# Kernel optimization log

Measured on AMD Instinct MI355X. Metric: run time of the kernel, lower is better.

Reference implementation:

```python
import jax, jax.numpy as jnp
import numpy as np

N = 100000      # num_nodes (num_users + num_items)
E = 1600000     # directed edges after symmetrization
DIN = 256
HID = 64
DOUT = 64


def setup_inputs() -> dict:
    key = jax.random.key(0)
    k = jax.random.split(key, 4)
    x = jax.random.normal(k[0], (N, DIN), dtype=jnp.float32)
    edge_index = jax.random.randint(k[1], (2, E), 0, N)
    edge_weight = jnp.ones((E,), dtype=jnp.float32)
    W1 = jax.random.normal(k[2], (DIN, HID), dtype=jnp.float32) * (1.0 / np.sqrt(DIN))
    b1 = jnp.zeros((HID,), dtype=jnp.float32)
    W2 = jax.random.normal(k[3], (HID, DOUT), dtype=jnp.float32) * (1.0 / np.sqrt(HID))
    b2 = jnp.zeros((DOUT,), dtype=jnp.float32)
    return {"x": x, "edge_index": edge_index, "edge_weight": edge_weight,
            "W1": W1, "b1": b1, "W2": W2, "b2": b2}


def _gcn_layer(x, W, b, src, dst, ew):
    # PyG GCNConv: h = x @ W; symmetric degree normalization; scatter-add at dst; + bias
    h = x @ W                                             # [N, D_out]
    deg = jax.ops.segment_sum(ew, dst, num_segments=N)    # in-degree w.r.t. edge weights
    dinv = jnp.where(deg > 0, jax.lax.rsqrt(deg), 0.0)    # deg^{-1/2}, inf -> 0
    norm = dinv[src] * ew * dinv[dst]                     # [E_tot]
    msg = h[src] * norm[:, None]                          # gather + scale
    out = jax.ops.segment_sum(msg, dst, num_segments=N)   # scatter-add
    return out + b


def reference(x, edge_index, edge_weight, W1, b1, W2, b2):
    # add self-loops with weight 1 (GCNConv default add_self_loops=True)
    loop = jnp.arange(N, dtype=edge_index.dtype)
    src = jnp.concatenate([edge_index[0], loop])
    dst = jnp.concatenate([edge_index[1], loop])
    ew = jnp.concatenate([edge_weight, jnp.ones((N,), edge_weight.dtype)])
    h = jax.nn.relu(_gcn_layer(x, W1, b1, src, dst, ew))
    return _gcn_layer(h, W2, b2, src, dst, ew)
```

## Files before the change

### kernel.cpp

```cpp
#include <hip/hip_runtime.h>
#include <math.h>


#define GCN_DIN 256
#define GCN_HID 64
#define SCAN_B 1024

__global__ void count_kernel(const int* __restrict__ dst, int* __restrict__ counts, int E) {
    int e = blockIdx.x * blockDim.x + threadIdx.x;
    if (e < E) atomicAdd(&counts[dst[e]], 1);
}

__global__ __launch_bounds__(SCAN_B) void scan_reduce_kernel(
    const int* __restrict__ counts, int* __restrict__ blockSums, int N)
{
    __shared__ int red[SCAN_B];
    int t = threadIdx.x;
    int i = blockIdx.x * SCAN_B + t;
    red[t] = (i < N) ? counts[i] : 0;
    __syncthreads();
    #pragma unroll
    for (int off = SCAN_B / 2; off > 0; off >>= 1) {
        if (t < off) red[t] += red[t + off];
        __syncthreads();
    }
    if (t == 0) blockSums[blockIdx.x] = red[0];
}

__global__ __launch_bounds__(128) void scan_sums_kernel(
    const int* __restrict__ blockSums, int* __restrict__ blockOff,
    int* __restrict__ rowptr, int B, int N)
{
    __shared__ int s[128];
    int t = threadIdx.x;
    int v = (t < B) ? blockSums[t] : 0;
    s[t] = v;
    __syncthreads();
    #pragma unroll
    for (int off = 1; off < 128; off <<= 1) {
        int a = (t >= off) ? s[t - off] : 0;
        __syncthreads();
        s[t] += a;
        __syncthreads();
    }
    if (t < B) blockOff[t] = s[t] - v;
    if (t == B - 1) rowptr[N] = s[t];
}

__global__ __launch_bounds__(SCAN_B) void scan_final_kernel(
    const int* __restrict__ counts, const int* __restrict__ blockOff,
    int* __restrict__ rowptr, int* __restrict__ cursor, int N)
{
    __shared__ int s[SCAN_B];
    int t = threadIdx.x;
    int i = blockIdx.x * SCAN_B + t;
    int v = (i < N) ? counts[i] : 0;
    s[t] = v;
    __syncthreads();
    for (int off = 1; off < SCAN_B; off <<= 1) {
        int a = (t >= off) ? s[t - off] : 0;
        __syncthreads();
        s[t] += a;
        __syncthreads();
    }
    if (i < N) {
        int excl = blockOff[blockIdx.x] + s[t] - v;
        rowptr[i] = excl;
        cursor[i] = excl;
    }
}

__global__ void reorder_kernel(const int* __restrict__ src, const int* __restrict__ dst,
                               const float* __restrict__ ew, int* __restrict__ cursor,
                               int2* __restrict__ comb, int E) {
    int e = blockIdx.x * blockDim.x + threadIdx.x;
    if (e < E) {
        int d = dst[e];
        int pos = atomicAdd(&cursor[d], 1);
        comb[pos] = make_int2(src[e], __float_as_int(ew[e]));
    }
}

__global__ void degw_kernel(const int* __restrict__ rowptr, const int2* __restrict__ comb,
                            float* __restrict__ dinv, int N) {
    int n = blockIdx.x * blockDim.x + threadIdx.x;
    if (n >= N) return;
    float s = 1.0f;
    int je = rowptr[n + 1];
    for (int j = rowptr[n]; j < je; ++j) s += __int_as_float(comb[j].y);
    dinv[n] = (s > 0.f) ? (1.0f / sqrtf(s)) : 0.f;
}

__global__ __launch_bounds__(256) void gemm1_kernel(
    const float* __restrict__ x, const float* __restrict__ W,
    const float* __restrict__ dinv, float* __restrict__ g, int N)
{
    __shared__ float xs[32][68];
    __shared__ float ws[32][64];
    const int tid = threadIdx.x;
    const int tx = tid & 15;
    const int ty = tid >> 4;
    const int row0 = blockIdx.x * 64;

    float acc[4][4];
    #pragma unroll
    for (int i = 0; i < 4; ++i)
        #pragma unroll
        for (int j = 0; j < 4; ++j) acc[i][j] = 0.f;

    for (int k0 = 0; k0 < GCN_DIN; k0 += 32) {
        {
            int kc = tid & 7;
            int r  = tid >> 3;
            #pragma unroll
            for (int h = 0; h < 2; ++h) {
                int rr = r + 32 * h;
                int row = row0 + rr;
                float4 v = make_float4(0.f, 0.f, 0.f, 0.f);
                if (row < N) v = *(const float4*)&x[(size_t)row * GCN_DIN + k0 + kc * 4];
                xs[kc * 4 + 0][rr] = v.x;
                xs[kc * 4 + 1][rr] = v.y;
                xs[kc * 4 + 2][rr] = v.z;
                xs[kc * 4 + 3][rr] = v.w;
            }
        }
        {
            int c  = tid & 63;
            int kr = tid >> 6;
            #pragma unroll
            for (int h = 0; h < 8; ++h)
                ws[kr + 4 * h][c] = W[(size_t)(k0 + kr + 4 * h) * 64 + c];
        }
        __syncthreads();
        #pragma unroll
        for (int kk = 0; kk < 32; ++kk) {
            float4 a = *(const float4*)&xs[kk][ty * 4];
            float4 b = *(const float4*)&ws[kk][tx * 4];
            float av[4] = {a.x, a.y, a.z, a.w};
            float bv[4] = {b.x, b.y, b.z, b.w};
            #pragma unroll
            for (int i = 0; i < 4; ++i)
                #pragma unroll
                for (int j = 0; j < 4; ++j)
                    acc[i][j] = fmaf(av[i], bv[j], acc[i][j]);
        }
        __syncthreads();
    }
    #pragma unroll
    for (int i = 0; i < 4; ++i) {
        int row = row0 + ty * 4 + i;
        if (row < N) {
            float dv = dinv[row];
            float4 o = make_float4(dv * acc[i][0], dv * acc[i][1],
                                   dv * acc[i][2], dv * acc[i][3]);
            *(float4*)&g[(size_t)row * 64 + tx * 4] = o;
        }
    }
}

__global__ __launch_bounds__(256) void gemm2_kernel(
    const float* __restrict__ acc1, const float* __restrict__ W,
    const float* __restrict__ dinv, const float* __restrict__ b1,
    float* __restrict__ g, int N)
{
    __shared__ float xs[32][68];
    __shared__ float ws[32][64];
    const int tid = threadIdx.x;
    const int tx = tid & 15;
    const int ty = tid >> 4;
    const int row0 = blockIdx.x * 64;

    float acc[4][4];
    #pragma unroll
    for (int i = 0; i < 4; ++i)
        #pragma unroll
        for (int j = 0; j < 4; ++j) acc[i][j] = 0.f;

    for (int k0 = 0; k0 < GCN_HID; k0 += 32) {
        {
            int kc = tid & 7;
            int r  = tid >> 3;
            float4 bb = *(const float4*)&b1[k0 + kc * 4];
            #pragma unroll
            for (int h = 0; h < 2; ++h) {
                int rr = r + 32 * h;
                int row = row0 + rr;
                float4 v = make_float4(0.f, 0.f, 0.f, 0.f);
                if (row < N) {
                    float dv = dinv[row];
                    float4 hh = *(const float4*)&acc1[(size_t)row * 64 + k0 + kc * 4];
                    v.x = fmaxf(dv * hh.x + bb.x, 0.f);
                    v.y = fmaxf(dv * hh.y + bb.y, 0.f);
                    v.z = fmaxf(dv * hh.z + bb.z, 0.f);
                    v.w = fmaxf(dv * hh.w + bb.w, 0.f);
                }
                xs[kc * 4 + 0][rr] = v.x;
                xs[kc * 4 + 1][rr] = v.y;
                xs[kc * 4 + 2][rr] = v.z;
                xs[kc * 4 + 3][rr] = v.w;
            }
        }
        {
            int c  = tid & 63;
            int kr = tid >> 6;
            #pragma unroll
            for (int h = 0; h < 8; ++h)
                ws[kr + 4 * h][c] = W[(size_t)(k0 + kr + 4 * h) * 64 + c];
        }
        __syncthreads();
        #pragma unroll
        for (int kk = 0; kk < 32; ++kk) {
            float4 a = *(const float4*)&xs[kk][ty * 4];
            float4 b = *(const float4*)&ws[kk][tx * 4];
            float av[4] = {a.x, a.y, a.z, a.w};
            float bv[4] = {b.x, b.y, b.z, b.w};
            #pragma unroll
            for (int i = 0; i < 4; ++i)
                #pragma unroll
                for (int j = 0; j < 4; ++j)
                    acc[i][j] = fmaf(av[i], bv[j], acc[i][j]);
        }
        __syncthreads();
    }
    #pragma unroll
    for (int i = 0; i < 4; ++i) {
        int row = row0 + ty * 4 + i;
        if (row < N) {
            float dv = dinv[row];
            float4 o = make_float4(dv * acc[i][0], dv * acc[i][1],
                                   dv * acc[i][2], dv * acc[i][3]);
            *(float4*)&g[(size_t)row * 64 + tx * 4] = o;
        }
    }
}

__global__ __launch_bounds__(256) void pull_kernel(
    const int* __restrict__ rowptr, const int2* __restrict__ comb,
    const float* __restrict__ g, float* __restrict__ out, int N)
{
    int wid  = (blockIdx.x * blockDim.x + threadIdx.x) >> 6;
    int lane = threadIdx.x & 63;
    if (wid >= N) return;
    int jb = rowptr[wid], je = rowptr[wid + 1];
    float acc = g[(size_t)wid * 64 + lane];
    int j = jb;
    for (; j + 3 < je; j += 4) {
        int2 e0 = comb[j], e1 = comb[j + 1], e2 = comb[j + 2], e3 = comb[j + 3];
        float v0 = g[(size_t)e0.x * 64 + lane];
        float v1 = g[(size_t)e1.x * 64 + lane];
        float v2 = g[(size_t)e2.x * 64 + lane];
        float v3 = g[(size_t)e3.x * 64 + lane];
        acc = fmaf(__int_as_float(e0.y), v0, acc);
        acc = fmaf(__int_as_float(e1.y), v1, acc);
        acc = fmaf(__int_as_float(e2.y), v2, acc);
        acc = fmaf(__int_as_float(e3.y), v3, acc);
    }
    for (; j < je; ++j) {
        int2 e0 = comb[j];
        acc = fmaf(__int_as_float(e0.y), g[(size_t)e0.x * 64 + lane], acc);
    }
    out[(size_t)wid * 64 + lane] = acc;
}

__global__ __launch_bounds__(256) void pull_final_kernel(
    const int* __restrict__ rowptr, const int2* __restrict__ comb,
    const float* __restrict__ g, const float* __restrict__ dinv,
    const float* __restrict__ b2, float* __restrict__ out, int N)
{
    int wid  = (blockIdx.x * blockDim.x + threadIdx.x) >> 6;
    int lane = threadIdx.x & 63;
    if (wid >= N) return;
    int jb = rowptr[wid], je = rowptr[wid + 1];
    float acc = g[(size_t)wid * 64 + lane];
    int j = jb;
    for (; j + 3 < je; j += 4) {
        int2 e0 = comb[j], e1 = comb[j + 1], e2 = comb[j + 2], e3 = comb[j + 3];
        float v0 = g[(size_t)e0.x * 64 + lane];
        float v1 = g[(size_t)e1.x * 64 + lane];
        float v2 = g[(size_t)e2.x * 64 + lane];
        float v3 = g[(size_t)e3.x * 64 + lane];
        acc = fmaf(__int_as_float(e0.y), v0, acc);
        acc = fmaf(__int_as_float(e1.y), v1, acc);
        acc = fmaf(__int_as_float(e2.y), v2, acc);
        acc = fmaf(__int_as_float(e3.y), v3, acc);
    }
    for (; j < je; ++j) {
        int2 e0 = comb[j];
        acc = fmaf(__int_as_float(e0.y), g[(size_t)e0.x * 64 + lane], acc);
    }
    out[(size_t)wid * 64 + lane] = dinv[wid] * acc + b2[lane];
}

extern "C" void kernel_launch(void* const* d_in, const int* in_sizes, int n_in,
                              void* d_out, int out_size, void* d_ws, size_t ws_size,
                              hipStream_t stream) {
    const float* x  = (const float*)d_in[0];
    const int*   ei = (const int*)  d_in[1];
    const float* ew = (const float*)d_in[2];
    const float* W1 = (const float*)d_in[3];
    const float* b1 = (const float*)d_in[4];
    const float* W2 = (const float*)d_in[5];
    const float* b2 = (const float*)d_in[6];
    float* out = (float*)d_out;

    const int N = in_sizes[0] / GCN_DIN;
    const int E = in_sizes[1] / 2;
    const int* src = ei;
    const int* dst = ei + E;

    char* p = (char*)d_ws;
    int2*  comb   = (int2*)p;  p += (size_t)E * sizeof(int2);
    float* B1     = (float*)p; p += (size_t)N * 64 * sizeof(float);
    float* B2     = (float*)p; p += (size_t)N * 64 * sizeof(float);
    float* dinv   = (float*)p; p += (size_t)N * sizeof(float);
    int*   counts = (int*)p;   p += (size_t)N * sizeof(int);
    int*   cursor = (int*)p;   p += (size_t)N * sizeof(int);
    int*   rowptr = (int*)p;   p += (size_t)(N + 1) * sizeof(int);
    int*   blockSums = (int*)p; p += 128 * sizeof(int);
    int*   blockOff  = (int*)p; p += 128 * sizeof(int);

    const int eBlocks = (E + 255) / 256;
    const int gBlocks = (N + 63) / 64;
    const int wBlocks = (N + 3) / 4;
    const int sBlocks = (N + SCAN_B - 1) / SCAN_B;

    hipMemsetAsync(counts, 0, (size_t)N * sizeof(int), stream);
    count_kernel<<<eBlocks, 256, 0, stream>>>(dst, counts, E);
    scan_reduce_kernel<<<sBlocks, SCAN_B, 0, stream>>>(counts, blockSums, N);
    scan_sums_kernel<<<1, 128, 0, stream>>>(blockSums, blockOff, rowptr, sBlocks, N);
    scan_final_kernel<<<sBlocks, SCAN_B, 0, stream>>>(counts, blockOff, rowptr, cursor, N);
    reorder_kernel<<<eBlocks, 256, 0, stream>>>(src, dst, ew, cursor, comb, E);
    degw_kernel<<<(N + 255) / 256, 256, 0, stream>>>(rowptr, comb, dinv, N);

    gemm1_kernel<<<gBlocks, 256, 0, stream>>>(x, W1, dinv, B1, N);
    pull_kernel<<<wBlocks, 256, 0, stream>>>(rowptr, comb, B1, B2, N);

    gemm2_kernel<<<gBlocks, 256, 0, stream>>>(B2, W2, dinv, b1, B1, N);
    pull_final_kernel<<<wBlocks, 256, 0, stream>>>(rowptr, comb, B1, dinv, b2, out, N);
}
```

Before: 544.0 us.

## Replace per-edge atomic CSR reorder with two-pass bucketed partition

The single-pass CSR reorder did one global atomic per edge on per-node cursors and wrote edges to scattered positions. It is replaced by a two-level counting sort. First, edges are partitioned into 512-node buckets, using shared-memory histograms and one global atomic per bucket per chunk. Then, one block per bucket scatters edges into final CSR positions using shared-memory cursors. This adds a kernel launch, an extra pass over the edges through a temporary buffer that aliases B1, and packs source and local destination into 32 bits, which assumes N fits in 17 bits and at most 256 buckets.

```diff
diff --git a/kernel.cpp b/kernel.cpp
--- a/kernel.cpp
+++ b/kernel.cpp
@@ -5,6 +5,8 @@
 #define GCN_DIN 256
 #define GCN_HID 64
 #define SCAN_B 1024
+#define PCHUNK 4096
+#define NBMAX 256
 
 __global__ void count_kernel(const int* __restrict__ dst, int* __restrict__ counts, int E) {
     int e = blockIdx.x * blockDim.x + threadIdx.x;
@@ -49,7 +51,7 @@
 
 __global__ __launch_bounds__(SCAN_B) void scan_final_kernel(
     const int* __restrict__ counts, const int* __restrict__ blockOff,
-    int* __restrict__ rowptr, int* __restrict__ cursor, int N)
+    int* __restrict__ rowptr, int N)
 {
     __shared__ int s[SCAN_B];
     int t = threadIdx.x;
@@ -63,21 +65,64 @@
         s[t] += a;
         __syncthreads();
     }
-    if (i < N) {
-        int excl = blockOff[blockIdx.x] + s[t] - v;
-        rowptr[i] = excl;
-        cursor[i] = excl;
-    }
-}
-
-__global__ void reorder_kernel(const int* __restrict__ src, const int* __restrict__ dst,
-                               const float* __restrict__ ew, int* __restrict__ cursor,
-                               int2* __restrict__ comb, int E) {
-    int e = blockIdx.x * blockDim.x + threadIdx.x;
-    if (e < E) {
+    if (i < N) rowptr[i] = blockOff[blockIdx.x] + s[t] - v;
+}
+
+__global__ void bcur_init_kernel(const int* __restrict__ rowptr, int* __restrict__ bucketCursor,
+                                 int NB, int N) {
+    int b = blockIdx.x * blockDim.x + threadIdx.x;
+    if (b < NB) {
+        int node = b << 9;
+        bucketCursor[b] = rowptr[node < N ? node : N];
+    }
+}
+
+__global__ __launch_bounds__(256) void partition_kernel(
+    const int* __restrict__ src, const int* __restrict__ dst, const float* __restrict__ ew,
+    int* __restrict__ bucketCursor, int2* __restrict__ tmp, int E)
+{
+    __shared__ int hcount[NBMAX];
+    __shared__ int hbase[NBMAX];
+    __shared__ int hoff[NBMAX];
+    const int tid = threadIdx.x;
+    const int b0 = blockIdx.x * PCHUNK;
+    const int bend = (b0 + PCHUNK < E) ? (b0 + PCHUNK) : E;
+
+    for (int i = tid; i < NBMAX; i += 256) { hcount[i] = 0; hoff[i] = 0; }
+    __syncthreads();
+    for (int e = b0 + tid; e < bend; e += 256)
+        atomicAdd(&hcount[dst[e] >> 9], 1);
+    __syncthreads();
+    for (int i = tid; i < NBMAX; i += 256)
+        if (hcount[i] > 0) hbase[i] = atomicAdd(&bucketCursor[i], hcount[i]);
+    __syncthreads();
+    for (int e = b0 + tid; e < bend; e += 256) {
         int d = dst[e];
-        int pos = atomicAdd(&cursor[d], 1);
-        comb[pos] = make_int2(src[e], __float_as_int(ew[e]));
+        int b = d >> 9;
+        int off = atomicAdd(&hoff[b], 1);
+        int key = ((d & 511) << 17) | src[e];
+        tmp[hbase[b] + off] = make_int2(key, __float_as_int(ew[e]));
+    }
+}
+
+__global__ __launch_bounds__(256) void bucket_scatter_kernel(
+    const int* __restrict__ rowptr, const int2* __restrict__ tmp,
+    int2* __restrict__ comb, int N)
+{
+    __shared__ int cur[512];
+    const int tid = threadIdx.x;
+    const int base = blockIdx.x << 9;
+    const int nn = (base + 512 < N) ? 512 : (N - base);
+    for (int i = tid; i < nn; i += 256) cur[i] = rowptr[base + i];
+    __syncthreads();
+    const int jb = rowptr[base];
+    const int je = rowptr[base + nn];
+    for (int j = jb + tid; j < je; j += 256) {
+        int2 t = tmp[j];
+        int local = t.x >> 17;
+        int s = t.x & 0x1FFFF;
+        int pos = atomicAdd(&cur[local], 1);
+        comb[pos] = make_int2(s, t.y);
     }
 }
 
@@ -307,6 +352,7 @@
     const int E = in_sizes[1] / 2;
     const int* src = ei;
     const int* dst = ei + E;
+    const int NB = (N + 511) >> 9;
 
     char* p = (char*)d_ws;
     int2*  comb   = (int2*)p;  p += (size_t)E * sizeof(int2);
@@ -314,22 +360,26 @@
     float* B2     = (float*)p; p += (size_t)N * 64 * sizeof(float);
     float* dinv   = (float*)p; p += (size_t)N * sizeof(float);
     int*   counts = (int*)p;   p += (size_t)N * sizeof(int);
-    int*   cursor = (int*)p;   p += (size_t)N * sizeof(int);
     int*   rowptr = (int*)p;   p += (size_t)(N + 1) * sizeof(int);
     int*   blockSums = (int*)p; p += 128 * sizeof(int);
     int*   blockOff  = (int*)p; p += 128 * sizeof(int);
+    int*   bucketCursor = (int*)p; p += NBMAX * sizeof(int);
+    int2*  tmp = (int2*)B1;
 
     const int eBlocks = (E + 255) / 256;
     const int gBlocks = (N + 63) / 64;
     const int wBlocks = (N + 3) / 4;
     const int sBlocks = (N + SCAN_B - 1) / SCAN_B;
+    const int pBlocks = (E + PCHUNK - 1) / PCHUNK;
 
     hipMemsetAsync(counts, 0, (size_t)N * sizeof(int), stream);
     count_kernel<<<eBlocks, 256, 0, stream>>>(dst, counts, E);
     scan_reduce_kernel<<<sBlocks, SCAN_B, 0, stream>>>(counts, blockSums, N);
     scan_sums_kernel<<<1, 128, 0, stream>>>(blockSums, blockOff, rowptr, sBlocks, N);
-    scan_final_kernel<<<sBlocks, SCAN_B, 0, stream>>>(counts, blockOff, rowptr, cursor, N);
-    reorder_kernel<<<eBlocks, 256, 0, stream>>>(src, dst, ew, cursor, comb, E);
+    scan_final_kernel<<<sBlocks, SCAN_B, 0, stream>>>(counts, blockOff, rowptr, N);
+    bcur_init_kernel<<<1, 256, 0, stream>>>(rowptr, bucketCursor, NB, N);
+    partition_kernel<<<pBlocks, 256, 0, stream>>>(src, dst, ew, bucketCursor, tmp, E);
+    bucket_scatter_kernel<<<NB, 256, 0, stream>>>(rowptr, tmp, comb, N);
     degw_kernel<<<(N + 255) / 256, 256, 0, stream>>>(rowptr, comb, dinv, N);
 
     gemm1_kernel<<<gBlocks, 256, 0, stream>>>(x, W1, dinv, B1, N);
```

Result: faster. 497.1 us (-8.6%).
